# Performance work log

Measured on AMD Instinct MI355X. Metric: run time of the kernel, lower is better.

The kernel has to match this reference:

```python
import jax, jax.numpy as jnp
import numpy as np

N_NODES = 50000
N_EDGES = 800000
NODE_DIM = 64
EDGE_DIM = 32
HIDDEN_DIM = 128
OUT_DIM = 64


def setup_inputs() -> dict:
    key = jax.random.key(0)
    k1, k2, k3, k4, k5, k6, k7 = jax.random.split(key, 7)
    in_dim = EDGE_DIM + 2 * NODE_DIM  # 160
    edge_index = jax.random.randint(k1, (2, N_EDGES), 0, N_NODES, dtype=jnp.int64)
    node_features = jax.random.normal(k2, (N_NODES, NODE_DIM), dtype=jnp.float32)
    edge_features = jax.random.normal(k3, (N_EDGES, EDGE_DIM), dtype=jnp.float32)
    # MLP params (kaiming-uniform-ish init scale, values only matter for correctness testing)
    w1 = jax.random.normal(k4, (in_dim, HIDDEN_DIM), dtype=jnp.float32) * (1.0 / np.sqrt(in_dim))
    b1 = jax.random.normal(k5, (HIDDEN_DIM,), dtype=jnp.float32) * 0.01
    w2 = jax.random.normal(k6, (HIDDEN_DIM, OUT_DIM), dtype=jnp.float32) * (1.0 / np.sqrt(HIDDEN_DIM))
    b2 = jax.random.normal(k7, (OUT_DIM,), dtype=jnp.float32) * 0.01
    return {
        "edge_index": edge_index,
        "node_features": node_features,
        "edge_features": edge_features,
        "w1": w1, "b1": b1, "w2": w2, "b2": b2,
    }


def reference(edge_index, node_features, edge_features, w1, b1, w2, b2):
    # Gather source / target node features along the edge list: [E, NODE_DIM]
    src = node_features[edge_index[0]]
    tgt = node_features[edge_index[1]]
    # Concat to [E, EDGE_DIM + 2*NODE_DIM]
    x = jnp.concatenate([edge_features, src, tgt], axis=1)
    # 2-layer MLP: Linear -> ReLU -> Linear
    h = jax.nn.relu(x @ w1 + b1)
    return h @ w2 + b2
```

## Files before the change

### kernel.cpp

```cpp
#include <hip/hip_runtime.h>

#define E_TOTAL 800000
#define NN      50000
#define ND      64
#define ED      32
#define HD      128
#define OD      64
#define IND     160
#define MT      128
#define NTHREADS 512

typedef __attribute__((ext_vector_type(8))) short          short8;
typedef __attribute__((ext_vector_type(4))) float          f32x4;
typedef __attribute__((ext_vector_type(8))) unsigned short u16x8;
typedef __attribute__((ext_vector_type(4))) unsigned short u16x4;

__device__ __forceinline__ unsigned short f2bf(float f) {
  union { float f; unsigned u; } v; v.f = f;
  unsigned r = v.u + 0x7fffu + ((v.u >> 16) & 1u);
  return (unsigned short)(r >> 16);
}

#define H_FRAGS  32
#define SMEM_U16 ((H_FRAGS + 40) * 512)
#define SMEM_BYTES (SMEM_U16 * 2)

__global__ void cvt_nodes(const float* __restrict__ in, unsigned short* __restrict__ out, int n4) {
  int i = blockIdx.x * blockDim.x + threadIdx.x;
  const int stride = gridDim.x * blockDim.x;
  for (; i < n4; i += stride) {
    float4 v = ((const float4*)in)[i];
    u16x4 o = { f2bf(v.x), f2bf(v.y), f2bf(v.z), f2bf(v.w) };
    ((u16x4*)out)[i] = o;
  }
}

__global__ void pack_w1(const float* __restrict__ w, unsigned short* __restrict__ out) {
  int i = blockIdx.x * blockDim.x + threadIdx.x;
  if (i >= HD * IND) return;
  int j = i & 7, l = (i >> 3) & 63, f = i >> 9;
  int ks = f >> 3, t = f & 7;
  int k = ks * 32 + (l >> 4) * 8 + j;
  int n = t * 16 + (l & 15);
  out[i] = f2bf(w[k * HD + n]);
}

__global__ void pack_w2(const float* __restrict__ w, unsigned short* __restrict__ out) {
  int i = blockIdx.x * blockDim.x + threadIdx.x;
  if (i >= OD * HD) return;
  int j = i & 7, l = (i >> 3) & 63, f = i >> 9;
  int ks = f >> 2, t = f & 3;
  int k = ks * 32 + (l >> 4) * 8 + j;
  int n = t * 16 + (l & 15);
  out[i] = f2bf(w[k * OD + n]);
}

__global__ __launch_bounds__(NTHREADS, 4)
void edge_mlp(const int* __restrict__ eidx,
              const float* __restrict__ ef,
              const unsigned short* __restrict__ nbf,
              const unsigned short* __restrict__ w1p,
              const unsigned short* __restrict__ w2p,
              const float* __restrict__ b1,
              const float* __restrict__ b2,
              float* __restrict__ out)
{
  extern __shared__ unsigned short sm[];
  unsigned short* Hs = sm;
  unsigned short* W1 = sm + H_FRAGS * 512;

  const int tid  = threadIdx.x;
  const int wid  = tid >> 6;
  const int lane = tid & 63;
  const int lq   = lane >> 4;
  const int lr   = lane & 15;
  const long e   = (long)blockIdx.x * MT + wid * 16 + lr;

  int si = eidx[e];
  int ti = eidx[E_TOTAL + e];

  const float4 e0v = *(const float4*)(ef + e * ED + lq * 8);
  const float4 e1v = *(const float4*)(ef + e * ED + lq * 8 + 4);

  u16x8 wv[5];
  #pragma unroll
  for (int c = 0; c < 5; ++c)
    wv[c] = *(const u16x8*)(w1p + (tid + c * NTHREADS) * 8);

  float b1v[8];
  #pragma unroll
  for (int t = 0; t < 8; ++t) b1v[t] = b1[t * 16 + lr];
  float b2v[4];
  #pragma unroll
  for (int t = 0; t < 4; ++t) b2v[t] = b2[t * 16 + lr];

  si = si < 0 ? 0 : (si >= NN ? NN - 1 : si);
  ti = ti < 0 ? 0 : (ti >= NN ? NN - 1 : ti);
  const unsigned short* sr = nbf + (long)si * ND;
  const unsigned short* tr = nbf + (long)ti * ND;
  const short8 g0 = *(const short8*)(sr + lq * 8);
  const short8 g1 = *(const short8*)(sr + 32 + lq * 8);
  const short8 g2 = *(const short8*)(tr + lq * 8);
  const short8 g3 = *(const short8*)(tr + 32 + lq * 8);

  #pragma unroll
  for (int c = 0; c < 5; ++c)
    *(u16x8*)(W1 + (tid + c * NTHREADS) * 8) = wv[c];

  asm volatile("s_waitcnt lgkmcnt(0)" ::: "memory");
  __builtin_amdgcn_s_barrier();

  short8 aef;
  aef[0] = (short)f2bf(e0v.x); aef[1] = (short)f2bf(e0v.y);
  aef[2] = (short)f2bf(e0v.z); aef[3] = (short)f2bf(e0v.w);
  aef[4] = (short)f2bf(e1v.x); aef[5] = (short)f2bf(e1v.y);
  aef[6] = (short)f2bf(e1v.z); aef[7] = (short)f2bf(e1v.w);

  f32x4 acc[8];
  #pragma unroll
  for (int t = 0; t < 8; ++t) acc[t] = (f32x4)0.0f;

  #define L1STEP(AV, KS)                                                        \
    _Pragma("unroll")                                                           \
    for (int t = 0; t < 8; ++t) {                                               \
      const short8 b = *(const short8*)(W1 + ((KS) * 8 + t) * 512 + lane * 8);  \
      acc[t] = __builtin_amdgcn_mfma_f32_16x16x32_bf16(AV, b, acc[t], 0, 0, 0); \
    }
  L1STEP(g0, 1)
  L1STEP(g1, 2)
  L1STEP(g2, 3)
  L1STEP(g3, 4)
  L1STEP(aef, 0)
  #undef L1STEP

  #pragma unroll
  for (int t = 0; t < 8; ++t) {
    #pragma unroll
    for (int r = 0; r < 4; ++r) {
      float h = acc[t][r] + b1v[t];
      h = h > 0.0f ? h : 0.0f;
      const int k    = t * 16 + lr;
      const int frag = wid * 4 + (k >> 5);
      const int l2   = (((k >> 3) & 3) << 4) + lq * 4 + r;
      Hs[frag * 512 + l2 * 8 + (k & 7)] = f2bf(h);
    }
  }

  short8 a2[4];
  #pragma unroll
  for (int ks = 0; ks < 4; ++ks)
    a2[ks] = *(const short8*)(Hs + (wid * 4 + ks) * 512 + lane * 8);

  f32x4 acc2[4];
  #pragma unroll
  for (int t = 0; t < 4; ++t) acc2[t] = (f32x4)0.0f;
  #pragma unroll
  for (int t = 0; t < 4; ++t) {
    #pragma unroll
    for (int ks = 0; ks < 4; ++ks) {
      const short8 b = *(const short8*)(w2p + ((ks * 4 + t) * 64 + lane) * 8);
      acc2[t] = __builtin_amdgcn_mfma_f32_16x16x32_bf16(a2[ks], b, acc2[t], 0, 0, 0);
    }
  }

  const long mbase = (long)blockIdx.x * MT + wid * 16 + lq * 4;
  #pragma unroll
  for (int t = 0; t < 4; ++t) {
    #pragma unroll
    for (int r = 0; r < 4; ++r) {
      out[(mbase + r) * OD + t * 16 + lr] = acc2[t][r] + b2v[t];
    }
  }
}

extern "C" void kernel_launch(void* const* d_in, const int* in_sizes, int n_in,
                              void* d_out, int out_size, void* d_ws, size_t ws_size,
                              hipStream_t stream) {
  const int*   eidx = (const int*)d_in[0];
  const float* nf   = (const float*)d_in[1];
  const float* ef   = (const float*)d_in[2];
  const float* w1   = (const float*)d_in[3];
  const float* b1   = (const float*)d_in[4];
  const float* w2   = (const float*)d_in[5];
  const float* b2   = (const float*)d_in[6];
  float*       out  = (float*)d_out;

  unsigned short* nbf = (unsigned short*)d_ws;
  unsigned short* w1p = nbf + (long)NN * ND;
  unsigned short* w2p = w1p + (long)HD * IND;

  cvt_nodes<<<1024, 256, 0, stream>>>(nf, nbf, (NN * ND) / 4);
  pack_w1<<<(HD * IND + 255) / 256, 256, 0, stream>>>(w1, w1p);
  pack_w2<<<(OD * HD + 255) / 256, 256, 0, stream>>>(w2, w2p);

  hipFuncSetAttribute((const void*)edge_mlp,
                      hipFuncAttributeMaxDynamicSharedMemorySize, SMEM_BYTES);
  edge_mlp<<<E_TOTAL / MT, NTHREADS, SMEM_BYTES, stream>>>(
      eidx, ef, nbf, w1p, w2p, b1, b2, out);
}
```

Measured before the change: 132.4 us.

## Process two 128-edge tiles per block with all gathers issued up front

Each block now handles 256 edges as two 128-edge sub-tiles. All index, edge-feature and node-feature gathers for both sub-tiles are issued before the shared W1 staging and barrier, and the two MLP passes then run one after the other. This spreads the per-block cost of copying W1 into shared memory over twice the work and keeps more global loads in flight to hide gather latency. In exchange, per-thread register use rises, which could cause spills or lower occupancy, and the grid has half as many blocks.

```diff
diff --git a/kernel.cpp b/kernel.cpp
--- a/kernel.cpp
+++ b/kernel.cpp
@@ -7,7 +7,7 @@
 #define HD      128
 #define OD      64
 #define IND     160
-#define MT      128
+#define MT2     256
 #define NTHREADS 512
 
 typedef __attribute__((ext_vector_type(8))) short          short8;
@@ -74,13 +74,18 @@
   const int lane = tid & 63;
   const int lq   = lane >> 4;
   const int lr   = lane & 15;
-  const long e   = (long)blockIdx.x * MT + wid * 16 + lr;
-
-  int si = eidx[e];
-  int ti = eidx[E_TOTAL + e];
-
-  const float4 e0v = *(const float4*)(ef + e * ED + lq * 8);
-  const float4 e1v = *(const float4*)(ef + e * ED + lq * 8 + 4);
+  const long eA  = (long)blockIdx.x * MT2 + wid * 16 + lr;
+  const long eB  = eA + 128;
+
+  int siA = eidx[eA];
+  int tiA = eidx[E_TOTAL + eA];
+  int siB = eidx[eB];
+  int tiB = eidx[E_TOTAL + eB];
+
+  const float4 evA0 = *(const float4*)(ef + eA * ED + lq * 8);
+  const float4 evA1 = *(const float4*)(ef + eA * ED + lq * 8 + 4);
+  const float4 evB0 = *(const float4*)(ef + eB * ED + lq * 8);
+  const float4 evB1 = *(const float4*)(ef + eB * ED + lq * 8 + 4);
 
   u16x8 wv[5];
   #pragma unroll
@@ -94,83 +99,96 @@
   #pragma unroll
   for (int t = 0; t < 4; ++t) b2v[t] = b2[t * 16 + lr];
 
-  si = si < 0 ? 0 : (si >= NN ? NN - 1 : si);
-  ti = ti < 0 ? 0 : (ti >= NN ? NN - 1 : ti);
-  const unsigned short* sr = nbf + (long)si * ND;
-  const unsigned short* tr = nbf + (long)ti * ND;
-  const short8 g0 = *(const short8*)(sr + lq * 8);
-  const short8 g1 = *(const short8*)(sr + 32 + lq * 8);
-  const short8 g2 = *(const short8*)(tr + lq * 8);
-  const short8 g3 = *(const short8*)(tr + 32 + lq * 8);
+  siA = siA < 0 ? 0 : (siA >= NN ? NN - 1 : siA);
+  tiA = tiA < 0 ? 0 : (tiA >= NN ? NN - 1 : tiA);
+  siB = siB < 0 ? 0 : (siB >= NN ? NN - 1 : siB);
+  tiB = tiB < 0 ? 0 : (tiB >= NN ? NN - 1 : tiB);
+  const unsigned short* srA = nbf + (long)siA * ND;
+  const unsigned short* trA = nbf + (long)tiA * ND;
+  const unsigned short* srB = nbf + (long)siB * ND;
+  const unsigned short* trB = nbf + (long)tiB * ND;
+  const short8 gA0 = *(const short8*)(srA + lq * 8);
+  const short8 gA1 = *(const short8*)(srA + 32 + lq * 8);
+  const short8 gA2 = *(const short8*)(trA + lq * 8);
+  const short8 gA3 = *(const short8*)(trA + 32 + lq * 8);
+  const short8 gB0 = *(const short8*)(srB + lq * 8);
+  const short8 gB1 = *(const short8*)(srB + 32 + lq * 8);
+  const short8 gB2 = *(const short8*)(trB + lq * 8);
+  const short8 gB3 = *(const short8*)(trB + 32 + lq * 8);
 
   #pragma unroll
   for (int c = 0; c < 5; ++c)
     *(u16x8*)(W1 + (tid + c * NTHREADS) * 8) = wv[c];
 
+  __builtin_amdgcn_sched_barrier(0);
+
   asm volatile("s_waitcnt lgkmcnt(0)" ::: "memory");
   __builtin_amdgcn_s_barrier();
 
-  short8 aef;
-  aef[0] = (short)f2bf(e0v.x); aef[1] = (short)f2bf(e0v.y);
-  aef[2] = (short)f2bf(e0v.z); aef[3] = (short)f2bf(e0v.w);
-  aef[4] = (short)f2bf(e1v.x); aef[5] = (short)f2bf(e1v.y);
-  aef[6] = (short)f2bf(e1v.z); aef[7] = (short)f2bf(e1v.w);
-
-  f32x4 acc[8];
-  #pragma unroll
-  for (int t = 0; t < 8; ++t) acc[t] = (f32x4)0.0f;
-
-  #define L1STEP(AV, KS)                                                        \
+  #define L1STEP(AV, KS, ACC)                                                   \
     _Pragma("unroll")                                                           \
     for (int t = 0; t < 8; ++t) {                                               \
       const short8 b = *(const short8*)(W1 + ((KS) * 8 + t) * 512 + lane * 8);  \
-      acc[t] = __builtin_amdgcn_mfma_f32_16x16x32_bf16(AV, b, acc[t], 0, 0, 0); \
+      ACC[t] = __builtin_amdgcn_mfma_f32_16x16x32_bf16(AV, b, ACC[t], 0, 0, 0); \
     }
-  L1STEP(g0, 1)
-  L1STEP(g1, 2)
-  L1STEP(g2, 3)
-  L1STEP(g3, 4)
-  L1STEP(aef, 0)
+
+  #define COMPUTE(G0, G1, G2, G3, EV0, EV1, MB)                                 \
+    {                                                                           \
+      f32x4 acc[8];                                                             \
+      _Pragma("unroll")                                                         \
+      for (int t = 0; t < 8; ++t) acc[t] = (f32x4)0.0f;                         \
+      L1STEP(G0, 1, acc)                                                        \
+      L1STEP(G1, 2, acc)                                                        \
+      L1STEP(G2, 3, acc)                                                        \
+      L1STEP(G3, 4, acc)                                                        \
+      short8 aef;                                                               \
+      aef[0] = (short)f2bf(EV0.x); aef[1] = (short)f2bf(EV0.y);                 \
+      aef[2] = (short)f2bf(EV0.z); aef[3] = (short)f2bf(EV0.w);                 \
+      aef[4] = (short)f2bf(EV1.x); aef[5] = (short)f2bf(EV1.y);                 \
+      aef[6] = (short)f2bf(EV1.z); aef[7] = (short)f2bf(EV1.w);                 \
+      L1STEP(aef, 0, acc)                                                       \
+      _Pragma("unroll")                                                         \
+      for (int t = 0; t < 8; ++t) {                                             \
+        _Pragma("unroll")                                                       \
+        for (int r = 0; r < 4; ++r) {                                           \
+          float h = acc[t][r] + b1v[t];                                         \
+          h = h > 0.0f ? h : 0.0f;                                              \
+          const int k    = t * 16 + lr;                                         \
+          const int frag = wid * 4 + (k >> 5);                                  \
+          const int l2   = (((k >> 3) & 3) << 4) + lq * 4 + r;                  \
+          Hs[frag * 512 + l2 * 8 + (k & 7)] = f2bf(h);                          \
+        }                                                                       \
+      }                                                                         \
+      short8 a2[4];                                                             \
+      _Pragma("unroll")                                                         \
+      for (int ks = 0; ks < 4; ++ks)                                            \
+        a2[ks] = *(const short8*)(Hs + (wid * 4 + ks) * 512 + lane * 8);        \
+      f32x4 acc2[4];                                                            \
+      _Pragma("unroll")                                                         \
+      for (int t = 0; t < 4; ++t) acc2[t] = (f32x4)0.0f;                        \
+      _Pragma("unroll")                                                         \
+      for (int t = 0; t < 4; ++t) {                                             \
+        _Pragma("unroll")                                                       \
+        for (int ks = 0; ks < 4; ++ks) {                                        \
+          const short8 b = *(const short8*)(w2p + ((ks * 4 + t) * 64 + lane) * 8); \
+          acc2[t] = __builtin_amdgcn_mfma_f32_16x16x32_bf16(a2[ks], b, acc2[t], 0, 0, 0); \
+        }                                                                       \
+      }                                                                         \
+      const long mbase = (MB) + wid * 16 + lq * 4;                              \
+      _Pragma("unroll")                                                         \
+      for (int t = 0; t < 4; ++t) {                                             \
+        _Pragma("unroll")                                                       \
+        for (int r = 0; r < 4; ++r) {                                           \
+          out[(mbase + r) * OD + t * 16 + lr] = acc2[t][r] + b2v[t];            \
+        }                                                                       \
+      }                                                                         \
+    }
+
+  COMPUTE(gA0, gA1, gA2, gA3, evA0, evA1, (long)blockIdx.x * MT2)
+  COMPUTE(gB0, gB1, gB2, gB3, evB0, evB1, (long)blockIdx.x * MT2 + 128)
+
+  #undef COMPUTE
   #undef L1STEP
-
-  #pragma unroll
-  for (int t = 0; t < 8; ++t) {
-    #pragma unroll
-    for (int r = 0; r < 4; ++r) {
-      float h = acc[t][r] + b1v[t];
-      h = h > 0.0f ? h : 0.0f;
-      const int k    = t * 16 + lr;
-      const int frag = wid * 4 + (k >> 5);
-      const int l2   = (((k >> 3) & 3) << 4) + lq * 4 + r;
-      Hs[frag * 512 + l2 * 8 + (k & 7)] = f2bf(h);
-    }
-  }
-
-  short8 a2[4];
-  #pragma unroll
-  for (int ks = 0; ks < 4; ++ks)
-    a2[ks] = *(const short8*)(Hs + (wid * 4 + ks) * 512 + lane * 8);
-
-  f32x4 acc2[4];
-  #pragma unroll
-  for (int t = 0; t < 4; ++t) acc2[t] = (f32x4)0.0f;
-  #pragma unroll
-  for (int t = 0; t < 4; ++t) {
-    #pragma unroll
-    for (int ks = 0; ks < 4; ++ks) {
-      const short8 b = *(const short8*)(w2p + ((ks * 4 + t) * 64 + lane) * 8);
-      acc2[t] = __builtin_amdgcn_mfma_f32_16x16x32_bf16(a2[ks], b, acc2[t], 0, 0, 0);
-    }
-  }
-
-  const long mbase = (long)blockIdx.x * MT + wid * 16 + lq * 4;
-  #pragma unroll
-  for (int t = 0; t < 4; ++t) {
-    #pragma unroll
-    for (int r = 0; r < 4; ++r) {
-      out[(mbase + r) * OD + t * 16 + lr] = acc2[t][r] + b2v[t];
-    }
-  }
 }
 
 extern "C" void kernel_launch(void* const* d_in, const int* in_sizes, int n_in,
@@ -195,6 +213,6 @@
 
   hipFuncSetAttribute((const void*)edge_mlp,
                       hipFuncAttributeMaxDynamicSharedMemorySize, SMEM_BYTES);
-  edge_mlp<<<E_TOTAL / MT, NTHREADS, SMEM_BYTES, stream>>>(
+  edge_mlp<<<E_TOTAL / MT2, NTHREADS, SMEM_BYTES, stream>>>(
       eidx, ef, nbf, w1p, w2p, b1, b2, out);
 }
```

New measurement: 138.7 us. 1.05x slower.

## Transpose MFMA operands so outputs are row-contiguous; shrink H scratch and raise occupancy

Applied to the files above, without the earlier changes.

Swaps the A/B operands of both MFMA layers so each lane's accumulator holds four consecutive output columns of one edge. This allows float4 output stores and packed bf16 pair writes into a small per-wave padded scratch in place of the scattered per-element hidden-layer stores. The second layer is interleaved per K-slice with the hidden-layer conversion. LDS use shrinks, launch bounds rise from 4 to 6 blocks per CU, and bias loads become vector loads at use time. The risk is that the higher occupancy target squeezes registers and causes spills.

```diff
diff --git a/kernel.cpp b/kernel.cpp
--- a/kernel.cpp
+++ b/kernel.cpp
@@ -14,6 +14,7 @@
 typedef __attribute__((ext_vector_type(4))) float          f32x4;
 typedef __attribute__((ext_vector_type(8))) unsigned short u16x8;
 typedef __attribute__((ext_vector_type(4))) unsigned short u16x4;
+typedef __attribute__((ext_vector_type(2))) unsigned int   u32x2;
 
 __device__ __forceinline__ unsigned short f2bf(float f) {
   union { float f; unsigned u; } v; v.f = f;
@@ -21,9 +22,9 @@
   return (unsigned short)(r >> 16);
 }
 
-#define H_FRAGS  32
-#define SMEM_U16 ((H_FRAGS + 40) * 512)
-#define SMEM_BYTES (SMEM_U16 * 2)
+#define W1_FRAGS 40
+#define SCR_DW_WAVE 320
+#define SMEM_BYTES (W1_FRAGS * 1024 + 8 * SCR_DW_WAVE * 4)
 
 __global__ void cvt_nodes(const float* __restrict__ in, unsigned short* __restrict__ out, int n4) {
   int i = blockIdx.x * blockDim.x + threadIdx.x;
@@ -55,7 +56,7 @@
   out[i] = f2bf(w[k * OD + n]);
 }
 
-__global__ __launch_bounds__(NTHREADS, 4)
+__global__ __launch_bounds__(NTHREADS, 6)
 void edge_mlp(const int* __restrict__ eidx,
               const float* __restrict__ ef,
               const unsigned short* __restrict__ nbf,
@@ -66,8 +67,8 @@
               float* __restrict__ out)
 {
   extern __shared__ unsigned short sm[];
-  unsigned short* Hs = sm;
-  unsigned short* W1 = sm + H_FRAGS * 512;
+  unsigned short* W1 = sm;
+  unsigned int*   Hs = (unsigned int*)(sm + W1_FRAGS * 512);
 
   const int tid  = threadIdx.x;
   const int wid  = tid >> 6;
@@ -86,13 +87,6 @@
   #pragma unroll
   for (int c = 0; c < 5; ++c)
     wv[c] = *(const u16x8*)(w1p + (tid + c * NTHREADS) * 8);
-
-  float b1v[8];
-  #pragma unroll
-  for (int t = 0; t < 8; ++t) b1v[t] = b1[t * 16 + lr];
-  float b2v[4];
-  #pragma unroll
-  for (int t = 0; t < 4; ++t) b2v[t] = b2[t * 16 + lr];
 
   si = si < 0 ? 0 : (si >= NN ? NN - 1 : si);
   ti = ti < 0 ? 0 : (ti >= NN ? NN - 1 : ti);
@@ -120,11 +114,11 @@
   #pragma unroll
   for (int t = 0; t < 8; ++t) acc[t] = (f32x4)0.0f;
 
-  #define L1STEP(AV, KS)                                                        \
+  #define L1STEP(BV, KS)                                                        \
     _Pragma("unroll")                                                           \
-    for (int t = 0; t < 8; ++t) {                                               \
-      const short8 b = *(const short8*)(W1 + ((KS) * 8 + t) * 512 + lane * 8);  \
-      acc[t] = __builtin_amdgcn_mfma_f32_16x16x32_bf16(AV, b, acc[t], 0, 0, 0); \
+    for (int nt = 0; nt < 8; ++nt) {                                            \
+      const short8 a = *(const short8*)(W1 + ((KS) * 8 + nt) * 512 + lane * 8); \
+      acc[nt] = __builtin_amdgcn_mfma_f32_16x16x32_bf16(a, BV, acc[nt], 0, 0, 0); \
     }
   L1STEP(g0, 1)
   L1STEP(g1, 2)
@@ -133,43 +127,43 @@
   L1STEP(aef, 0)
   #undef L1STEP
 
+  unsigned int* scr = Hs + wid * SCR_DW_WAVE;
+  f32x4 acc2[4];
   #pragma unroll
-  for (int t = 0; t < 8; ++t) {
+  for (int t = 0; t < 4; ++t) acc2[t] = (f32x4)0.0f;
+
+  #pragma unroll
+  for (int ks = 0; ks < 4; ++ks) {
     #pragma unroll
-    for (int r = 0; r < 4; ++r) {
-      float h = acc[t][r] + b1v[t];
-      h = h > 0.0f ? h : 0.0f;
-      const int k    = t * 16 + lr;
-      const int frag = wid * 4 + (k >> 5);
-      const int l2   = (((k >> 3) & 3) << 4) + lq * 4 + r;
-      Hs[frag * 512 + l2 * 8 + (k & 7)] = f2bf(h);
+    for (int h = 0; h < 2; ++h) {
+      const int nt = 2 * ks + h;
+      const float4 bq = *(const float4*)(b1 + nt * 16 + lq * 4);
+      const float h0 = fmaxf(acc[nt][0] + bq.x, 0.0f);
+      const float h1 = fmaxf(acc[nt][1] + bq.y, 0.0f);
+      const float h2 = fmaxf(acc[nt][2] + bq.z, 0.0f);
+      const float h3 = fmaxf(acc[nt][3] + bq.w, 0.0f);
+      u32x2 wpair;
+      wpair[0] = (unsigned)f2bf(h0) | ((unsigned)f2bf(h1) << 16);
+      wpair[1] = (unsigned)f2bf(h2) | ((unsigned)f2bf(h3) << 16);
+      *(u32x2*)(scr + lr * 20 + 8 * h + lq * 2) = wpair;
+    }
+    const short8 a2 = *(const short8*)((const unsigned short*)(scr + lr * 20 + lq * 4));
+    #pragma unroll
+    for (int t = 0; t < 4; ++t) {
+      const short8 wa = *(const short8*)(w2p + ((ks * 4 + t) * 64 + lane) * 8);
+      acc2[t] = __builtin_amdgcn_mfma_f32_16x16x32_bf16(wa, a2, acc2[t], 0, 0, 0);
     }
   }
 
-  short8 a2[4];
-  #pragma unroll
-  for (int ks = 0; ks < 4; ++ks)
-    a2[ks] = *(const short8*)(Hs + (wid * 4 + ks) * 512 + lane * 8);
-
-  f32x4 acc2[4];
-  #pragma unroll
-  for (int t = 0; t < 4; ++t) acc2[t] = (f32x4)0.0f;
   #pragma unroll
   for (int t = 0; t < 4; ++t) {
-    #pragma unroll
-    for (int ks = 0; ks < 4; ++ks) {
-      const short8 b = *(const short8*)(w2p + ((ks * 4 + t) * 64 + lane) * 8);
-      acc2[t] = __builtin_amdgcn_mfma_f32_16x16x32_bf16(a2[ks], b, acc2[t], 0, 0, 0);
-    }
-  }
-
-  const long mbase = (long)blockIdx.x * MT + wid * 16 + lq * 4;
-  #pragma unroll
-  for (int t = 0; t < 4; ++t) {
-    #pragma unroll
-    for (int r = 0; r < 4; ++r) {
-      out[(mbase + r) * OD + t * 16 + lr] = acc2[t][r] + b2v[t];
-    }
+    const float4 bq = *(const float4*)(b2 + t * 16 + lq * 4);
+    float4 o;
+    o.x = acc2[t][0] + bq.x;
+    o.y = acc2[t][1] + bq.y;
+    o.z = acc2[t][2] + bq.z;
+    o.w = acc2[t][3] + bq.w;
+    *(float4*)(out + e * OD + t * 16 + lq * 4) = o;
   }
 }
 
```

Result: slower. 145.5 us (+9.9%).
